# Kernel optimization log

Hardware: AMD Instinct MI355X
Metric: run time of the kernel (lower is better)

## Reference

```python
import jax, jax.numpy as jnp
import numpy as np

LAMBDA = 20.0   # lambda_val (blackbox-diff smoothing)
REG = 0.5       # reg
MAX_LABEL = 8   # labels drawn in [0, MAX_LABEL)


def _pairwise_dist(x):
    # x: [n, d] -> [n, n] euclidean distances (safe sqrt, exact 0 on diagonal)
    sq = jnp.sum(x * x, axis=-1)
    d2 = sq[:, None] + sq[None, :] - 2.0 * (x @ x.T)
    d2 = jnp.maximum(d2, 0.0)
    return jnp.where(d2 > 0, jnp.sqrt(jnp.where(d2 > 0, d2, 1.0)), 0.0)


def _single_linkage_adj(D, k):
    # Agglomerative (single-linkage) clustering of n points given [n,n] dists,
    # stopped at k clusters; returns [n,n] 0/1 cluster-adjacency matrix.
    n = D.shape[0]
    BIG = jnp.asarray(1e9, D.dtype)
    eye = jnp.eye(n, dtype=bool)
    Dw0 = jnp.where(eye, BIG, D)
    labels0 = jnp.arange(n)
    active0 = jnp.ones((n,), dtype=bool)

    def step(carry, _):
        Dw, labels, active = carry
        mask = active[:, None] & active[None, :] & ~eye
        flat = jnp.argmin(jnp.where(mask, Dw, BIG))
        i, j = flat // n, flat % n
        a = jnp.minimum(i, j)
        b = jnp.maximum(i, j)
        newrow = jnp.minimum(Dw[a], Dw[b])        # single linkage merge
        Dw = Dw.at[a, :].set(newrow).at[:, a].set(newrow)
        active = active.at[b].set(False)
        labels = jnp.where(labels == b, a, labels)
        return (Dw, labels, active), labels

    _, hist = jax.lax.scan(step, (Dw0, labels0, active0), None, length=n - 1)
    all_hist = jnp.concatenate([labels0[None, :], hist], axis=0)  # [n, n]; row m = labels after m merges (n-m clusters)
    lab = all_hist[n - k]
    return (lab[:, None] == lab[None, :]).astype(D.dtype)


def _solve(dists, ks):
    return jax.vmap(_single_linkage_adj)(dists, ks)


def setup_inputs() -> dict:
    key = jax.random.key(0)
    k1, k2, k3 = jax.random.split(key, 3)
    B, n, d = 256, 64, 768
    return {
        "query_embedding": jax.random.normal(k1, (B, d), dtype=jnp.float32),
        "psg_embeddings": jax.random.normal(k2, (B, n, d), dtype=jnp.float32),
        "labels": jax.random.randint(k3, (B, n), 0, MAX_LABEL, dtype=jnp.int64)
        if jax.config.jax_enable_x64 else jax.random.randint(k3, (B, n), 0, MAX_LABEL, dtype=jnp.int32),
    }


def reference(query_embedding, psg_embeddings, labels):
    # true_adj_mat: adj[i,j] = 1 iff i==j or label[i]==label[j] (diag is label-equal anyway)
    true_adj = (labels[:, :, None] == labels[:, None, :]).astype(jnp.float32)  # [B,n,n]
    # ks[i] = number of unique labels in sample i
    presence = (labels[..., None] == jnp.arange(MAX_LABEL)).any(axis=1)  # [B, MAX_LABEL]
    ks = presence.sum(axis=-1)

    scaled = query_embedding[:, None, :] * psg_embeddings            # [B,n,d]
    dists = jax.vmap(_pairwise_dist)(scaled)                          # [B,n,n]

    mean_similar = (dists * true_adj).sum() / true_adj.sum()
    mean_dissimilar = (dists * (1.0 - true_adj)).sum() / (1.0 - true_adj).sum()

    adj = _solve(dists, ks)                                           # OptimCluster forward
    err = adj * (1.0 - true_adj) + (1.0 - adj) * true_adj
    err_mean = err.mean(axis=0).sum()
    return err_mean + REG * (mean_similar - mean_dissimilar)
```

## Files before the change

kernel.cpp:

```cpp
#include <hip/hip_runtime.h>


#define NPTS 64
#define DIM 768
#define CH 128
#define NCH 6
#define NT 512
#define BIGF 1e9f
#define PGS 68

typedef __attribute__((ext_vector_type(8))) __bf16 bf16x8;
typedef __attribute__((ext_vector_type(4))) float f32x4;
typedef __attribute__((ext_vector_type(8))) unsigned short us8;

__device__ __forceinline__ void lds_fence() {
  asm volatile("s_waitcnt lgkmcnt(0)" ::: "memory");
  __builtin_amdgcn_sched_barrier(0);
}

__device__ __forceinline__ void split3(float x, unsigned short& h,
                                       unsigned short& m, unsigned short& l) {
  unsigned u = __float_as_uint(x);
  unsigned rb = (u + 0x7FFFu + ((u >> 16) & 1u)) & 0xFFFF0000u;
  h = (unsigned short)(rb >> 16);
  float r1 = x - __uint_as_float(rb);
  unsigned u1 = __float_as_uint(r1);
  unsigned rb1 = (u1 + 0x7FFFu + ((u1 >> 16) & 1u)) & 0xFFFF0000u;
  m = (unsigned short)(rb1 >> 16);
  float r2 = r1 - __uint_as_float(rb1);
  l = (unsigned short)(__float_as_uint(r2) >> 16);
}

__device__ __forceinline__ void stage_chunk(
    unsigned short (*Hb)[NPTS][CH], const float4 (&pva)[2][2],
    const float4 (&qv)[2], int row0, int gran) {
  #pragma unroll
  for (int rr = 0; rr < 2; ++rr) {
    const int row = row0 + (rr << 5);
    float xs[8];
    xs[0] = pva[rr][0].x * qv[0].x; xs[1] = pva[rr][0].y * qv[0].y;
    xs[2] = pva[rr][0].z * qv[0].z; xs[3] = pva[rr][0].w * qv[0].w;
    xs[4] = pva[rr][1].x * qv[1].x; xs[5] = pva[rr][1].y * qv[1].y;
    xs[6] = pva[rr][1].z * qv[1].z; xs[7] = pva[rr][1].w * qv[1].w;
    us8 uh, um, ul;
    #pragma unroll
    for (int e = 0; e < 8; ++e) {
      unsigned short hh, mm, ll;
      split3(xs[e], hh, mm, ll);
      uh[e] = hh; um[e] = mm; ul[e] = ll;
    }
    const int p = gran ^ (row & 15);
    *reinterpret_cast<us8*>(&Hb[0][row][p << 3]) = uh;
    *reinterpret_cast<us8*>(&Hb[1][row][p << 3]) = um;
    *reinterpret_cast<us8*>(&Hb[2][row][p << 3]) = ul;
  }
}

__device__ __forceinline__ void mfma_chunk(
    const unsigned short (*Hb)[NPTS][CH], f32x4 (&acc)[2][2],
    int R, int C, int ksub, int lrow, int lhi) {
  #pragma unroll 1
  for (int ss = 0; ss < 2; ++ss) {
    const int s = ksub + (ss << 1);
    const int p = ((s << 2) + lhi) ^ lrow;
    bf16x8 fa[3][2], fb[3][2];
    #pragma unroll
    for (int v = 0; v < 3; ++v)
      #pragma unroll
      for (int tb = 0; tb < 2; ++tb) {
        const int row = (R << 5) + (tb << 4) + lrow;
        fa[v][tb] = *reinterpret_cast<const bf16x8*>(&Hb[v][row][p << 3]);
      }
    if (R != C) {
      #pragma unroll
      for (int v = 0; v < 3; ++v)
        #pragma unroll
        for (int tb = 0; tb < 2; ++tb) {
          const int row = (C << 5) + (tb << 4) + lrow;
          fb[v][tb] = *reinterpret_cast<const bf16x8*>(&Hb[v][row][p << 3]);
        }
    } else {
      #pragma unroll
      for (int v = 0; v < 3; ++v)
        #pragma unroll
        for (int tb = 0; tb < 2; ++tb) fb[v][tb] = fa[v][tb];
    }
    #pragma unroll
    for (int ti = 0; ti < 2; ++ti)
      #pragma unroll
      for (int tj = 0; tj < 2; ++tj) {
        acc[ti][tj] = __builtin_amdgcn_mfma_f32_16x16x32_bf16(fa[0][ti], fb[0][tj], acc[ti][tj], 0, 0, 0);
        acc[ti][tj] = __builtin_amdgcn_mfma_f32_16x16x32_bf16(fa[0][ti], fb[1][tj], acc[ti][tj], 0, 0, 0);
        acc[ti][tj] = __builtin_amdgcn_mfma_f32_16x16x32_bf16(fa[1][ti], fb[0][tj], acc[ti][tj], 0, 0, 0);
        acc[ti][tj] = __builtin_amdgcn_mfma_f32_16x16x32_bf16(fa[1][ti], fb[1][tj], acc[ti][tj], 0, 0, 0);
        acc[ti][tj] = __builtin_amdgcn_mfma_f32_16x16x32_bf16(fa[0][ti], fb[2][tj], acc[ti][tj], 0, 0, 0);
        acc[ti][tj] = __builtin_amdgcn_mfma_f32_16x16x32_bf16(fa[2][ti], fb[0][tj], acc[ti][tj], 0, 0, 0);
      }
  }
}

#define ISSUE_P(PV, cix) do {                                       \
    const int off_ = (cix) * CH;                                    \
    PV[0][0] = *(const float4*)(pr0 + off_);                        \
    PV[0][1] = *(const float4*)(pr0 + off_ + 4);                    \
    PV[1][0] = *(const float4*)(pr1 + off_);                        \
    PV[1][1] = *(const float4*)(pr1 + off_ + 4);                    \
  } while (0)

#define ISSUE_Q(QV, cix) do {                                       \
    const int off_ = (cix) * CH;                                    \
    QV[0] = *(const float4*)(qr + off_);                            \
    QV[1] = *(const float4*)(qr + off_ + 4);                        \
  } while (0)

__global__ __launch_bounds__(NT) void fused_kernel(
    const float* __restrict__ q,
    const float* __restrict__ psg,
    const int*   __restrict__ labels,
    float* __restrict__ simS_o, float* __restrict__ disS_o,
    int* __restrict__ simC_o, int* __restrict__ errC_o)
{
  __shared__ __align__(16) unsigned short Hml[2][3][NPTS][CH];
  __shared__ __align__(16) float PG[NPTS * PGS];
  __shared__ float diagf[NPTS];
  __shared__ __align__(16) int cls[NPTS];
  __shared__ __align__(16) int comp_s[NPTS];
  __shared__ unsigned bw_s[NPTS], bfl_s[NPTS];
  __shared__ int ptr_s[NPTS], lab_s[NPTS];
  __shared__ __align__(8) unsigned long long ekey_s[NPTS];
  __shared__ int ecnt_s;

  const int b = blockIdx.x;
  const int t = threadIdx.x;
  const int w = t >> 6;
  const int l = t & 63;

  const float* qb = q + (size_t)b * DIM;
  const float* pb = psg + (size_t)b * NPTS * DIM;

  const int row0 = t >> 4;
  const int gran = t & 15;
  const float* pr0 = pb + (size_t)row0 * DIM + (gran << 3);
  const float* pr1 = pr0 + 32 * DIM;
  const float* qr  = qb + (gran << 3);

  const int rw = w >> 1;
  const int R = rw >> 1, C = rw & 1;
  const int ksub = w & 1;
  const int lrow = l & 15;
  const int lhi  = l >> 4;

  f32x4 acc[2][2];
  {
    f32x4 z = {0.f, 0.f, 0.f, 0.f};
    acc[0][0] = z; acc[0][1] = z; acc[1][0] = z; acc[1][1] = z;
  }

  float4 pvaA[2][2], pvaB[2][2], qv[2];

  ISSUE_P(pvaA, 0);
  ISSUE_Q(qv, 0);
  ISSUE_P(pvaB, 1);
  stage_chunk(Hml[0], pvaA, qv, row0, gran);
  __syncthreads();

  #pragma unroll 1
  for (int cc = 0; cc < 3; ++cc) {
    if (cc < 2) ISSUE_P(pvaA, 2 * cc + 2);
    ISSUE_Q(qv, 2 * cc + 1);
    mfma_chunk(Hml[0], acc, R, C, ksub, lrow, lhi);
    stage_chunk(Hml[1], pvaB, qv, row0, gran);
    __syncthreads();
    if (cc < 2) {
      ISSUE_P(pvaB, 2 * cc + 3);
      ISSUE_Q(qv, 2 * cc + 2);
    }
    mfma_chunk(Hml[1], acc, R, C, ksub, lrow, lhi);
    if (cc < 2) stage_chunk(Hml[0], pvaA, qv, row0, gran);
    __syncthreads();
  }

  if (w & 1) {
    float* dst = PG + (rw << 10);
    #pragma unroll
    for (int ti = 0; ti < 2; ++ti)
      #pragma unroll
      for (int tj = 0; tj < 2; ++tj)
        *reinterpret_cast<f32x4*>(dst + (((ti << 1) + tj) << 8) + (l << 2)) = acc[ti][tj];
  }
  __syncthreads();
  if (!(w & 1)) {
    const float* src = PG + (rw << 10);
    #pragma unroll
    for (int ti = 0; ti < 2; ++ti)
      #pragma unroll
      for (int tj = 0; tj < 2; ++tj)
        acc[ti][tj] += *reinterpret_cast<const f32x4*>(src + (((ti << 1) + tj) << 8) + (l << 2));
  }
  __syncthreads();
  if (!(w & 1)) {
    #pragma unroll
    for (int ti = 0; ti < 2; ++ti)
      #pragma unroll
      for (int tj = 0; tj < 2; ++tj)
        #pragma unroll
        for (int reg = 0; reg < 4; ++reg) {
          const int grow = (R << 5) + (ti << 4) + (lhi << 2) + reg;
          const int gcol = (C << 5) + (tj << 4) + lrow;
          PG[grow * PGS + gcol] = acc[ti][tj][reg];
        }
  }
  __syncthreads();

  if (t < NPTS) diagf[t] = PG[t * PGS + t];
  __syncthreads();
  {
    const int r  = t >> 3;
    const int c0 = (t & 7) << 3;
    const float dr = diagf[r];
    #pragma unroll
    for (int e = 0; e < 8; ++e) {
      const int cc = c0 + e;
      const float gg = PG[r * PGS + cc];
      float d2 = dr + diagf[cc] - 2.f * gg;
      d2 = fmaxf(d2, 0.f);
      PG[r * PGS + cc] = (d2 > 0.f) ? sqrtf(d2) : 0.f;
    }
  }
  __syncthreads();
  if (w != 0) return;

  float drow[64];
  #pragma unroll
  for (int v4 = 0; v4 < 16; ++v4) {
    f32x4 x = *reinterpret_cast<const f32x4*>(&PG[l * PGS + (v4 << 2)]);
    drow[v4 * 4 + 0] = x[0]; drow[v4 * 4 + 1] = x[1];
    drow[v4 * 4 + 2] = x[2]; drow[v4 * 4 + 3] = x[3];
  }
  int tl = labels[b * NPTS + l];

  unsigned long long sMask = 0ull;
  int kcnt = 0;
  #pragma unroll
  for (int v = 0; v < 8; ++v) {
    unsigned long long mv = __ballot(tl == v);
    kcnt += (mv != 0ull) ? 1 : 0;
    if (tl == v) sMask = mv;
  }
  int simC = __popcll(sMask);
  const int merges = NPTS - kcnt;

  float simS = 0.f, disS = 0.f;
  #pragma unroll
  for (int j = 0; j < NPTS; ++j) {
    bool sim = (sMask >> j) & 1ull;
    simS += sim ? drow[j] : 0.f;
    disS += sim ? 0.f : drow[j];
  }

  comp_s[l] = l; lab_s[l] = l;
  if (l == 0) ecnt_s = 0;
  lds_fence();

  #pragma unroll 1
  for (int rd = 0; rd < 6; ++rd) {
    bw_s[l] = 0xFFFFFFFFu; bfl_s[l] = 0xFFFFFFFFu;
    lds_fence();
    const int myc = comp_s[l];
    float bv = BIGF; int bj = 64;
    #pragma unroll
    for (int jc = 0; jc < 16; ++jc) {
      int4 c4 = *reinterpret_cast<const int4*>(&comp_s[jc << 2]);
      int cj[4] = {c4.x, c4.y, c4.z, c4.w};
      #pragma unroll
      for (int e = 0; e < 4; ++e) {
        const int j = (jc << 2) + e;
        bool ok = (cj[e] != myc) && (drow[j] < bv);
        bv = ok ? drow[j] : bv;
        bj = ok ? j : bj;
      }
    }
    if (bj < 64) atomicMin(&bw_s[myc], __float_as_uint(bv));
    lds_fence();
    unsigned bwc = bw_s[myc];
    if (bj < 64 && __float_as_uint(bv) == bwc)
      atomicMin(&bfl_s[myc], (unsigned)((l << 6) | bj));
    lds_fence();
    const bool isroot = (myc == l);
    const unsigned rw_ = bw_s[l];
    const unsigned rf  = bfl_s[l];
    int hook = l;
    if (isroot && rw_ != 0xFFFFFFFFu)
      hook = comp_s[rf & 63];
    ptr_s[l] = isroot ? hook : myc;
    lds_fence();
    if (isroot && hook != l) {
      const int pd = ptr_s[hook];
      if (pd == l && l < hook) {
        ptr_s[l] = l;
      } else {
        int slot = atomicAdd(&ecnt_s, 1);
        ekey_s[slot & 63] = ((unsigned long long)rw_ << 32) | (unsigned long long)rf;
      }
    }
    lds_fence();
    #pragma unroll 1
    for (int jj = 0; jj < 6; ++jj) {
      int pp = ptr_s[l];
      int p2 = ptr_s[pp & 63];
      if (__ballot(p2 != pp) == 0ull) break;
      ptr_s[l] = p2;
    }
    lds_fence();
    const int newc = ptr_s[l];
    comp_s[l] = newc;
    lds_fence();
    const int base = __shfl(newc, 0);
    if (__ballot(newc != base) == 0ull) break;
  }

  const int ec = ecnt_s;
  const bool ehave = (l < ec);
  const unsigned long long my = ehave ? ekey_s[l] : ~0ull;
  int rank = 0;
  #pragma unroll 7
  for (int j = 0; j < 63; ++j) {
    unsigned long long kj = ekey_s[j];
    rank += (j < ec && kj < my) ? 1 : 0;
  }
  const bool kept = ehave && (rank < merges);
  const int eu = (int)((my >> 6) & 63);
  const int ev = (int)(my & 63);

  #pragma unroll 1
  for (int iter = 0; iter < 64; ++iter) {
    int m = 0; bool ch = false;
    if (kept) {
      int lu = lab_s[eu], lv = lab_s[ev];
      m = min(lu, lv);
      ch = (m < lu) || (m < lv);
    }
    if (__ballot(ch) == 0ull) break;
    if (ch) {
      atomicMin(&lab_s[eu], m);
      atomicMin(&lab_s[ev], m);
    }
    lds_fence();
  }
  lds_fence();
  const int cl = lab_s[l];

  cls[l] = cl;
  lds_fence();
  unsigned long long cMask = 0ull;
  const int4* cp = reinterpret_cast<const int4*>(cls);
  #pragma unroll 4
  for (int jq = 0; jq < 16; ++jq) {
    int4 c4 = cp[jq];
    cMask |= ((unsigned long long)(c4.x == cl)) << (jq * 4 + 0);
    cMask |= ((unsigned long long)(c4.y == cl)) << (jq * 4 + 1);
    cMask |= ((unsigned long long)(c4.z == cl)) << (jq * 4 + 2);
    cMask |= ((unsigned long long)(c4.w == cl)) << (jq * 4 + 3);
  }
  int ec2 = __popcll(cMask ^ sMask);

  #pragma unroll
  for (int off = 32; off; off >>= 1) {
    simS += __shfl_xor(simS, off);
    disS += __shfl_xor(disS, off);
    simC += __shfl_xor(simC, off);
    ec2  += __shfl_xor(ec2, off);
  }
  if (l == 0) {
    simS_o[b] = simS; disS_o[b] = disS;
    simC_o[b] = simC; errC_o[b] = ec2;
  }
}

__global__ __launch_bounds__(64) void finalize_kernel(
    const float* __restrict__ simS, const float* __restrict__ disS,
    const int* __restrict__ simC, const int* __restrict__ errC,
    float* __restrict__ out)
{
  const int l = threadIdx.x;
  double ss = 0.0, dd = 0.0, sc = 0.0, ec = 0.0;
  #pragma unroll
  for (int r = 0; r < 4; ++r) {
    int i = (r << 6) + l;
    ss += (double)simS[i];
    dd += (double)disS[i];
    sc += (double)simC[i];
    ec += (double)errC[i];
  }
  #pragma unroll
  for (int off = 32; off; off >>= 1) {
    ss += __shfl_xor(ss, off);
    dd += __shfl_xor(dd, off);
    sc += __shfl_xor(sc, off);
    ec += __shfl_xor(ec, off);
  }
  if (l == 0) {
    const double total = 256.0 * 4096.0;
    double ms = ss / sc;
    double md = dd / (total - sc);
    out[0] = (float)(ec / 256.0 + 0.5 * (ms - md));
  }
}

extern "C" void kernel_launch(void* const* d_in, const int* in_sizes, int n_in,
                              void* d_out, int out_size, void* d_ws, size_t ws_size,
                              hipStream_t stream) {
  const float* q      = (const float*)d_in[0];
  const float* psg    = (const float*)d_in[1];
  const int*   labels = (const int*)d_in[2];
  float* out = (float*)d_out;

  float* simS = (float*)d_ws;
  float* disS = simS + 256;
  int*   simC = (int*)(disS + 256);
  int*   errC = simC + 256;

  fused_kernel<<<256, NT, 0, stream>>>(q, psg, labels, simS, disS, simC, errC);
  finalize_kernel<<<1, 64, 0, stream>>>(simS, disS, simC, errC, out);
}
```

Baseline: 32.41 us.

## Replace LDS-based Boruvka component tracking with wave-level ballots and shuffles

Component membership is now held as a 64-bit per-lane mask built by a six-ballot match, so the LDS comp_s, ptr_s, cls and ecnt_s arrays go away. Pointer jumping and edge-slot allocation use shuffles and ballot prefix counts instead of LDS reads and atomics. The label propagation loop gains a pointer-jump step per iteration to converge faster. Together these remove many LDS round trips and fences from the serial single-wave clustering phase, at the cost of more ballot and shuffle instructions.

```diff
diff --git a/kernel.cpp b/kernel.cpp
--- a/kernel.cpp
+++ b/kernel.cpp
@@ -31,6 +31,16 @@
   l = (unsigned short)(__float_as_uint(r2) >> 16);
 }
 
+__device__ __forceinline__ unsigned long long match6(int v) {
+  unsigned long long m = ~0ull;
+  #pragma unroll
+  for (int bb = 0; bb < 6; ++bb) {
+    unsigned long long mb = __ballot(((v >> bb) & 1) != 0);
+    m &= (((v >> bb) & 1) != 0) ? mb : ~mb;
+  }
+  return m;
+}
+
 __device__ __forceinline__ void stage_chunk(
     unsigned short (*Hb)[NPTS][CH], const float4 (&pva)[2][2],
     const float4 (&qv)[2], int row0, int gran) {
@@ -123,12 +133,9 @@
   __shared__ __align__(16) unsigned short Hml[2][3][NPTS][CH];
   __shared__ __align__(16) float PG[NPTS * PGS];
   __shared__ float diagf[NPTS];
-  __shared__ __align__(16) int cls[NPTS];
-  __shared__ __align__(16) int comp_s[NPTS];
   __shared__ unsigned bw_s[NPTS], bfl_s[NPTS];
-  __shared__ int ptr_s[NPTS], lab_s[NPTS];
+  __shared__ int lab_s[NPTS];
   __shared__ __align__(8) unsigned long long ekey_s[NPTS];
-  __shared__ int ecnt_s;
 
   const int b = blockIdx.x;
   const int t = threadIdx.x;
@@ -258,110 +265,93 @@
     disS += sim ? 0.f : drow[j];
   }
 
-  comp_s[l] = l; lab_s[l] = l;
-  if (l == 0) ecnt_s = 0;
-  lds_fence();
+  unsigned long long same = 1ull << l;
+  int repSlot = l;
+  int ecnt = 0;
 
   #pragma unroll 1
   for (int rd = 0; rd < 6; ++rd) {
     bw_s[l] = 0xFFFFFFFFu; bfl_s[l] = 0xFFFFFFFFu;
     lds_fence();
-    const int myc = comp_s[l];
     float bv = BIGF; int bj = 64;
     #pragma unroll
-    for (int jc = 0; jc < 16; ++jc) {
-      int4 c4 = *reinterpret_cast<const int4*>(&comp_s[jc << 2]);
-      int cj[4] = {c4.x, c4.y, c4.z, c4.w};
-      #pragma unroll
-      for (int e = 0; e < 4; ++e) {
-        const int j = (jc << 2) + e;
-        bool ok = (cj[e] != myc) && (drow[j] < bv);
-        bv = ok ? drow[j] : bv;
-        bj = ok ? j : bj;
-      }
-    }
-    if (bj < 64) atomicMin(&bw_s[myc], __float_as_uint(bv));
+    for (int j = 0; j < NPTS; ++j) {
+      bool ok = !((same >> j) & 1ull) && (drow[j] < bv);
+      bv = ok ? drow[j] : bv;
+      bj = ok ? j : bj;
+    }
+    if (bj < 64) atomicMin(&bw_s[repSlot], __float_as_uint(bv));
     lds_fence();
-    unsigned bwc = bw_s[myc];
+    const unsigned bwc = bw_s[repSlot];
     if (bj < 64 && __float_as_uint(bv) == bwc)
-      atomicMin(&bfl_s[myc], (unsigned)((l << 6) | bj));
+      atomicMin(&bfl_s[repSlot], (unsigned)((l << 6) | bj));
     lds_fence();
-    const bool isroot = (myc == l);
-    const unsigned rw_ = bw_s[l];
-    const unsigned rf  = bfl_s[l];
-    int hook = l;
-    if (isroot && rw_ != 0xFFFFFFFFu)
-      hook = comp_s[rf & 63];
-    ptr_s[l] = isroot ? hook : myc;
-    lds_fence();
-    if (isroot && hook != l) {
-      const int pd = ptr_s[hook];
-      if (pd == l && l < hook) {
-        ptr_s[l] = l;
-      } else {
-        int slot = atomicAdd(&ecnt_s, 1);
-        ekey_s[slot & 63] = ((unsigned long long)rw_ << 32) | (unsigned long long)rf;
-      }
-    }
-    lds_fence();
+    const unsigned rfl = bfl_s[repSlot];
+    const bool valid = (bwc != 0xFFFFFFFFu);
+    const int vpt = (int)(rfl & 63);
+    const int otherRep = __shfl(repSlot, vpt);
+    const bool isRoot = (l == repSlot);
+    int ptr = repSlot;
+    if (isRoot && valid) ptr = otherRep;
+    const int pd = __shfl(ptr, ptr);
+    bool adder = false;
+    if (isRoot && valid && ptr != l) {
+      if (pd == l && l < ptr) ptr = l;
+      else adder = true;
+    }
+    const unsigned long long A = __ballot(adder);
+    if (adder)
+      ekey_s[ecnt + __popcll(A & ((1ull << l) - 1ull))] =
+          ((unsigned long long)bwc << 12) | (unsigned long long)rfl;
+    ecnt += (int)__popcll(A);
     #pragma unroll 1
     for (int jj = 0; jj < 6; ++jj) {
-      int pp = ptr_s[l];
-      int p2 = ptr_s[pp & 63];
-      if (__ballot(p2 != pp) == 0ull) break;
-      ptr_s[l] = p2;
-    }
-    lds_fence();
-    const int newc = ptr_s[l];
-    comp_s[l] = newc;
-    lds_fence();
-    const int base = __shfl(newc, 0);
-    if (__ballot(newc != base) == 0ull) break;
-  }
-
-  const int ec = ecnt_s;
-  const bool ehave = (l < ec);
+      const int p2 = __shfl(ptr, ptr);
+      if (__ballot(p2 != ptr) == 0ull) break;
+      ptr = p2;
+    }
+    same = match6(ptr);
+    repSlot = __ffsll((long long)same) - 1;
+    if (same == ~0ull) break;
+  }
+  lds_fence();
+
+  const bool ehave = (l < ecnt);
   const unsigned long long my = ehave ? ekey_s[l] : ~0ull;
   int rank = 0;
   #pragma unroll 7
   for (int j = 0; j < 63; ++j) {
     unsigned long long kj = ekey_s[j];
-    rank += (j < ec && kj < my) ? 1 : 0;
+    rank += (j < ecnt && kj < my) ? 1 : 0;
   }
   const bool kept = ehave && (rank < merges);
   const int eu = (int)((my >> 6) & 63);
   const int ev = (int)(my & 63);
 
+  lab_s[l] = l;
+  lds_fence();
   #pragma unroll 1
   for (int iter = 0; iter < 64; ++iter) {
     int m = 0; bool ch = false;
     if (kept) {
-      int lu = lab_s[eu], lv = lab_s[ev];
+      const int lu = lab_s[eu], lv = lab_s[ev];
       m = min(lu, lv);
       ch = (m < lu) || (m < lv);
     }
-    if (__ballot(ch) == 0ull) break;
     if (ch) {
       atomicMin(&lab_s[eu], m);
       atomicMin(&lab_s[ev], m);
     }
     lds_fence();
-  }
-  lds_fence();
+    const int la = lab_s[l];
+    const int lb = lab_s[la];
+    if (lb < la) lab_s[l] = lb;
+    lds_fence();
+    if (__ballot(ch) == 0ull) break;
+  }
   const int cl = lab_s[l];
 
-  cls[l] = cl;
-  lds_fence();
-  unsigned long long cMask = 0ull;
-  const int4* cp = reinterpret_cast<const int4*>(cls);
-  #pragma unroll 4
-  for (int jq = 0; jq < 16; ++jq) {
-    int4 c4 = cp[jq];
-    cMask |= ((unsigned long long)(c4.x == cl)) << (jq * 4 + 0);
-    cMask |= ((unsigned long long)(c4.y == cl)) << (jq * 4 + 1);
-    cMask |= ((unsigned long long)(c4.z == cl)) << (jq * 4 + 2);
-    cMask |= ((unsigned long long)(c4.w == cl)) << (jq * 4 + 3);
-  }
+  const unsigned long long cMask = match6(cl);
   int ec2 = __popcll(cMask ^ sMask);
 
   #pragma unroll
```

After: 32.13 us. Within noise of the previous version (-0.9%).
